# Kernel optimization log

Hardware: AMD Instinct MI355X
Metric: run time of the kernel (lower is better)

## Reference

```python
import jax, jax.numpy as jnp
import numpy as np

N, M, T = 8, 4, 500000   # state dim, measurement dim, trajectory length
ITERS = 100


def setup_inputs() -> dict:
    key = jax.random.key(0)
    k1, k2, k3, k4 = jax.random.split(key, 4)
    xs = jax.random.normal(k1, (N, T), dtype=jnp.float32)
    ys = jax.random.normal(k2, (M, T), dtype=jnp.float32)
    # Well-conditioned, stable models: F near identity, modest H, SPD noise covs.
    F = jnp.eye(N, dtype=jnp.float32) + 0.01 * jax.random.normal(k3, (N, N), dtype=jnp.float32)
    H = 0.1 * jax.random.normal(k4, (M, N), dtype=jnp.float32)
    Q = jnp.eye(N, dtype=jnp.float32)
    R = jnp.eye(M, dtype=jnp.float32)
    gamma = jnp.float32(0.01)
    return {"xs": xs, "ys": ys, "F": F, "H": H, "Q": Q, "R": R, "gamma": gamma}


def reference(xs, ys, F, H, Q, R, gamma):
    # Precompute the message operators (done once in __init__ in the original).
    Qinv = jnp.linalg.inv(Q)
    Rinv = jnp.linalg.inv(R)
    negQinv = -Qinv            # n x n
    FtQinv = F.T @ Qinv        # n x n
    HtRinv = H.T @ Rinv        # n x m

    def step(x, _):
        # x: n x T. Shift columns to get x_{t-1} and x_{t+1} (edge-replicated).
        x_past = jnp.concatenate([x[:, :1], x[:, :-1]], axis=1)
        x_fut = jnp.concatenate([x[:, 1:], x[:, -1:]], axis=1)
        # diff_past_curr: x_t - F x_{t-1}, with ROW 0 zeroed (faithful to res[0]=0.0)
        d1 = (x - F @ x_past).at[0].set(0.0)
        # diff_curr_fut: x_{t+1} - F x_t, with LAST ROW zeroed (faithful to res[-1]=0.0)
        d2 = (x_fut - F @ x).at[-1].set(0.0)
        # diff_y_curr: y - H x_t
        d3 = ys - H @ x
        m = negQinv @ d1 + FtQinv @ d2 + HtRinv @ d3
        return x + gamma * m, None

    x, _ = jax.lax.scan(step, xs, None, length=ITERS)
    return x
```

## Files before the change

### kernel.cpp

```cpp
#include <hip/hip_runtime.h>

#define TLEN   500000
#define NITER  100
#define DHALF  6
#define NOFF   (2*DHALF+1)
#define STRIP  20
#define EWIN   32
#define CT     256
#define CCPT   4
#define NCONV  (((TLEN - 2*STRIP)/CCPT + CT - 1) / CT)
#define WROW   128

__global__ __launch_bounds__(256) void band_and_edges(
    const float* __restrict__ xs, const float* __restrict__ ys,
    const float* __restrict__ F, const float* __restrict__ H,
    const float* __restrict__ Q, const float* __restrict__ R,
    const float* __restrict__ gam,
    float* __restrict__ wout,
    float* __restrict__ out)
{
  __shared__ double dQaug[8][16];
  __shared__ double dRaug[4][8];
  __shared__ double dFtQi[64], dHtRi[32], dA1[64], dB2[64];
  __shared__ float fmats[224];
  __shared__ __align__(16) float st[2][34][8];

  const int tid = threadIdx.x;
  const int b   = blockIdx.x;
  const int r8  = (tid >> 3) & 7;
  const int c8  = tid & 7;

  if (tid < 64) {
    dQaug[r8][c8]     = (double)Q[r8*8 + c8];
    dQaug[r8][c8 + 8] = (c8 == r8) ? 1.0 : 0.0;
  } else if (tid < 96) {
    int t = tid - 64, rr = t >> 3, cr = t & 7;
    dRaug[rr][cr] = (cr < 4) ? (double)R[rr*4 + cr] : ((cr - 4 == rr) ? 1.0 : 0.0);
  }
  __syncthreads();
  for (int col = 0; col < 8; ++col) {
    double piv = 1, fq = 0, p1 = 0, p2 = 0, m1 = 0, m2 = 0;
    double rpiv = 1, frr = 0, pr = 0, mr = 0;
    const bool doQ = tid < 64;
    const bool doR = (tid >= 64 && tid < 96 && col < 4);
    if (doQ) {
      piv = dQaug[col][col]; fq = dQaug[r8][col];
      p1 = dQaug[col][c8];   p2 = dQaug[col][c8 + 8];
      m1 = dQaug[r8][c8];    m2 = dQaug[r8][c8 + 8];
    }
    if (doR) {
      int t = tid - 64, rr = t >> 3, cr = t & 7;
      rpiv = dRaug[col][col]; frr = dRaug[rr][col];
      pr = dRaug[col][cr];    mr = dRaug[rr][cr];
    }
    __syncthreads();
    if (doQ) {
      dQaug[r8][c8]     = (r8 == col) ? m1 / piv : m1 - fq * (p1 / piv);
      dQaug[r8][c8 + 8] = (r8 == col) ? m2 / piv : m2 - fq * (p2 / piv);
    }
    if (doR) {
      int t = tid - 64, rr = t >> 3, cr = t & 7;
      dRaug[rr][cr] = (rr == col) ? mr / rpiv : mr - frr * (pr / rpiv);
    }
    __syncthreads();
  }
  if (tid < 64) {
    double s = 0.0;
    #pragma unroll
    for (int k = 0; k < 8; ++k) s += (double)F[k*8 + r8] * dQaug[k][c8 + 8];
    dFtQi[r8*8 + c8] = s;
    dA1[r8*8 + c8] = (c8 == 0) ? 0.0 : -dQaug[r8][c8 + 8];
  } else if (tid < 96) {
    int t = tid - 64, i = t >> 2, j = t & 3;
    double s = 0.0;
    #pragma unroll
    for (int k = 0; k < 4; ++k) s += (double)H[k*8 + i] * dRaug[k][j + 4];
    dHtRi[i*4 + j] = s;
  }
  __syncthreads();
  if (tid < 64) dB2[r8*8 + c8] = (c8 == 7) ? 0.0 : dFtQi[r8*8 + c8];
  __syncthreads();
  {
    const double g = (double)gam[0];
    if (tid < 64) {
      double sp = 0.0;
      #pragma unroll
      for (int k = 0; k < 8; ++k) sp -= dA1[r8*8 + k] * (double)F[k*8 + c8];
      double t2 = dA1[r8*8 + c8];
      #pragma unroll
      for (int k = 0; k < 8; ++k) t2 -= dB2[r8*8 + k] * (double)F[k*8 + c8];
      #pragma unroll
      for (int k = 0; k < 4; ++k) t2 -= dHtRi[r8*4 + k] * (double)H[k*8 + c8];
      fmats[       c8*8 + r8] = (float)(((r8 == c8) ? 1.0 : 0.0) + g * t2);
      fmats[ 64 +  c8*8 + r8] = (float)(g * sp);
      fmats[128 +  c8*8 + r8] = (float)(g * dB2[r8*8 + c8]);
    } else if (tid < 96) {
      int t = tid - 64, i = t >> 2, j = t & 3;
      fmats[192 + j*8 + i] = (float)(g * dHtRi[i*4 + j]);
    }
  }
  __syncthreads();

  const int i = tid & 7;
  const int g = tid >> 3;
  float cmr[8], pmr[8], fur[7];
  #pragma unroll
  for (int k = 0; k < 8; ++k) {
    cmr[k] = fmats[       k*8 + i];
    pmr[k] = fmats[ 64 +  k*8 + i];
    if (k < 7) fur[k] = fmats[128 + k*8 + i];
  }
  float* const stf = (float*)st;
  const int BUF = 34*8;

  if (b < 12) {
    const int c = b;
    const bool act = tid < NOFF*8;
    const int s = g + 1;
    for (int idx = tid; idx < 2*BUF; idx += 256) stf[idx] = 0.0f;
    __syncthreads();
    if (act && c < 8 && s == DHALF + 1 && i == c) st[0][s][i] = 1.0f;
    const float seed = (act && c >= 8 && s == DHALF + 1) ? fmats[192 + (c - 8)*8 + i] : 0.0f;
    __syncthreads();
    int p = 0;
    float last = 0.0f;
    #pragma unroll 1
    for (int it = 0; it < NITER; ++it) {
      if (act) {
        const float* sp_ = stf + p*BUF;
        const float4 o0 = *(const float4*)(sp_ + s*8);
        const float4 o1 = *(const float4*)(sp_ + s*8 + 4);
        const float4 u0 = *(const float4*)(sp_ + (s + 1)*8);
        const float4 u1 = *(const float4*)(sp_ + (s + 1)*8 + 4);
        const float4 d0 = *(const float4*)(sp_ + (s - 1)*8);
        const float4 d1 = *(const float4*)(sp_ + (s - 1)*8 + 4);
        float a0 = seed, a1 = 0.0f, a2 = 0.0f;
        a0 = fmaf(cmr[0], o0.x, a0); a0 = fmaf(cmr[1], o0.y, a0);
        a0 = fmaf(cmr[2], o0.z, a0); a0 = fmaf(cmr[3], o0.w, a0);
        a0 = fmaf(cmr[4], o1.x, a0); a0 = fmaf(cmr[5], o1.y, a0);
        a0 = fmaf(cmr[6], o1.z, a0); a0 = fmaf(cmr[7], o1.w, a0);
        a1 = fmaf(pmr[0], u0.x, a1); a1 = fmaf(pmr[1], u0.y, a1);
        a1 = fmaf(pmr[2], u0.z, a1); a1 = fmaf(pmr[3], u0.w, a1);
        a1 = fmaf(pmr[4], u1.x, a1); a1 = fmaf(pmr[5], u1.y, a1);
        a1 = fmaf(pmr[6], u1.z, a1); a1 = fmaf(pmr[7], u1.w, a1);
        a2 = fmaf(fur[0], d0.x, a2); a2 = fmaf(fur[1], d0.y, a2);
        a2 = fmaf(fur[2], d0.z, a2); a2 = fmaf(fur[3], d0.w, a2);
        a2 = fmaf(fur[4], d1.x, a2); a2 = fmaf(fur[5], d1.y, a2);
        a2 = fmaf(fur[6], d1.z, a2);
        last = a0 + a1 + a2;
        stf[(p^1)*BUF + s*8 + i] = last;
      }
      __syncthreads();
      p ^= 1;
    }
    if (act) wout[c*WROW + (s - 1)*8 + i] = last;
    if (tid >= NOFF*8 && tid < WROW) wout[c*WROW + tid] = 0.0f;
    return;
  }

  const bool left = (b == 12);
  const int col  = g;
  const int gcol = left ? col : (TLEN - EWIN + col);
  const int sL = (col > 0) ? col - 1 : 0;
  const int sR = (col < EWIN - 1) ? col + 1 : EWIN - 1;
  const float xv = xs[i*TLEN + gcol];
  float gyv;
  {
    gyv = fmats[192 +      i] * ys[0*TLEN + gcol];
    gyv = fmaf(fmats[192 +  8 + i], ys[1*TLEN + gcol], gyv);
    gyv = fmaf(fmats[192 + 16 + i], ys[2*TLEN + gcol], gyv);
    gyv = fmaf(fmats[192 + 24 + i], ys[3*TLEN + gcol], gyv);
  }
  st[0][col][i] = xv;
  __syncthreads();
  int p = 0;
  float last = xv;
  #pragma unroll 1
  for (int it = 0; it < NITER; ++it) {
    const float* sp_ = stf + p*BUF;
    const float4 o0 = *(const float4*)(sp_ + col*8);
    const float4 o1 = *(const float4*)(sp_ + col*8 + 4);
    const float4 l0 = *(const float4*)(sp_ + sL*8);
    const float4 l1 = *(const float4*)(sp_ + sL*8 + 4);
    const float4 q0 = *(const float4*)(sp_ + sR*8);
    const float4 q1 = *(const float4*)(sp_ + sR*8 + 4);
    float a0 = gyv, a1 = 0.0f, a2 = 0.0f;
    a0 = fmaf(cmr[0], o0.x, a0); a0 = fmaf(cmr[1], o0.y, a0);
    a0 = fmaf(cmr[2], o0.z, a0); a0 = fmaf(cmr[3], o0.w, a0);
    a0 = fmaf(cmr[4], o1.x, a0); a0 = fmaf(cmr[5], o1.y, a0);
    a0 = fmaf(cmr[6], o1.z, a0); a0 = fmaf(cmr[7], o1.w, a0);
    a1 = fmaf(pmr[0], l0.x, a1); a1 = fmaf(pmr[1], l0.y, a1);
    a1 = fmaf(pmr[2], l0.z, a1); a1 = fmaf(pmr[3], l0.w, a1);
    a1 = fmaf(pmr[4], l1.x, a1); a1 = fmaf(pmr[5], l1.y, a1);
    a1 = fmaf(pmr[6], l1.z, a1); a1 = fmaf(pmr[7], l1.w, a1);
    a2 = fmaf(fur[0], q0.x, a2); a2 = fmaf(fur[1], q0.y, a2);
    a2 = fmaf(fur[2], q0.z, a2); a2 = fmaf(fur[3], q0.w, a2);
    a2 = fmaf(fur[4], q1.x, a2); a2 = fmaf(fur[5], q1.y, a2);
    a2 = fmaf(fur[6], q1.z, a2);
    last = a0 + a1 + a2;
    stf[(p^1)*BUF + col*8 + i] = last;
    __syncthreads();
    p ^= 1;
  }
  if (left ? (col < STRIP) : (col >= EWIN - STRIP)) out[i*TLEN + gcol] = last;
}

__global__ __launch_bounds__(CT) void kgm_conv(
    const float* __restrict__ xs, const float* __restrict__ ys,
    const float* __restrict__ wq, float* __restrict__ out)
{
  const int tid  = threadIdx.x;
  const int lane = tid & 63;
  const int ocol = STRIP + (blockIdx.x * CT + tid) * CCPT;
  const int col0 = (ocol <= TLEN - STRIP - CCPT) ? ocol : (TLEN - STRIP - CCPT);

  float4 acc[8];
  #pragma unroll
  for (int i = 0; i < 8; ++i) acc[i] = make_float4(0.f, 0.f, 0.f, 0.f);

  #pragma unroll 2
  for (int k = 0; k < 12; ++k) {
    const float* src = ((k < 8) ? (xs + k*TLEN) : (ys + (k-8)*TLEN)) + col0;
    const float wA = wq[k*WROW + lane];
    const float wB = wq[k*WROW + 64 + lane];
    float z[20];
    #pragma unroll
    for (int j = 0; j < 5; ++j) {
      float4 v = *(const float4*)(src - 8 + 4*j);
      z[4*j] = v.x; z[4*j + 1] = v.y; z[4*j + 2] = v.z; z[4*j + 3] = v.w;
    }
    #pragma unroll
    for (int d = 0; d < NOFF; ++d) {
      #pragma unroll
      for (int i = 0; i < 8; ++i) {
        constexpr int dummy = 0; (void)dummy;
        const int j = d*8 + i;
        const int wi = __builtin_amdgcn_readlane(
            __float_as_int((j < 64) ? wA : wB), j & 63);
        const float w = __int_as_float(wi);
        acc[i].x = fmaf(w, z[d + 2], acc[i].x);
        acc[i].y = fmaf(w, z[d + 3], acc[i].y);
        acc[i].z = fmaf(w, z[d + 4], acc[i].z);
        acc[i].w = fmaf(w, z[d + 5], acc[i].w);
      }
    }
  }

  if (ocol < TLEN - STRIP) {
    #pragma unroll
    for (int i = 0; i < 8; ++i)
      *(float4*)(out + i*TLEN + ocol) = acc[i];
  }
}

extern "C" void kernel_launch(void* const* d_in, const int* in_sizes, int n_in,
                              void* d_out, int out_size, void* d_ws, size_t ws_size,
                              hipStream_t stream)
{
  (void)in_sizes; (void)n_in; (void)out_size; (void)ws_size;
  const float* xs = (const float*)d_in[0];
  const float* ys = (const float*)d_in[1];
  const float* F  = (const float*)d_in[2];
  const float* H  = (const float*)d_in[3];
  const float* Q  = (const float*)d_in[4];
  const float* R  = (const float*)d_in[5];
  const float* ga = (const float*)d_in[6];
  float* ws  = (float*)d_ws;
  float* out = (float*)d_out;
  band_and_edges<<<14, 256, 0, stream>>>(xs, ys, F, H, Q, R, ga, ws, out);
  kgm_conv<<<NCONV, CT, 0, stream>>>(xs, ys, ws, out);
}
```

Before: 49.95 us.

## Double-buffer row loads and read convolution weights as uniform scalar loads

```diff
diff --git a/kernel.cpp b/kernel.cpp
--- a/kernel.cpp
+++ b/kernel.cpp
@@ -210,7 +210,6 @@
     const float* __restrict__ wq, float* __restrict__ out)
 {
   const int tid  = threadIdx.x;
-  const int lane = tid & 63;
   const int ocol = STRIP + (blockIdx.x * CT + tid) * CCPT;
   const int col0 = (ocol <= TLEN - STRIP - CCPT) ? ocol : (TLEN - STRIP - CCPT);
 
@@ -218,33 +217,47 @@
   #pragma unroll
   for (int i = 0; i < 8; ++i) acc[i] = make_float4(0.f, 0.f, 0.f, 0.f);
 
-  #pragma unroll 2
-  for (int k = 0; k < 12; ++k) {
-    const float* src = ((k < 8) ? (xs + k*TLEN) : (ys + (k-8)*TLEN)) + col0;
-    const float wA = wq[k*WROW + lane];
-    const float wB = wq[k*WROW + 64 + lane];
-    float z[20];
-    #pragma unroll
-    for (int j = 0; j < 5; ++j) {
-      float4 v = *(const float4*)(src - 8 + 4*j);
-      z[4*j] = v.x; z[4*j + 1] = v.y; z[4*j + 2] = v.z; z[4*j + 3] = v.w;
-    }
-    #pragma unroll
-    for (int d = 0; d < NOFF; ++d) {
-      #pragma unroll
-      for (int i = 0; i < 8; ++i) {
-        constexpr int dummy = 0; (void)dummy;
-        const int j = d*8 + i;
-        const int wi = __builtin_amdgcn_readlane(
-            __float_as_int((j < 64) ? wA : wB), j & 63);
-        const float w = __int_as_float(wi);
-        acc[i].x = fmaf(w, z[d + 2], acc[i].x);
-        acc[i].y = fmaf(w, z[d + 3], acc[i].y);
-        acc[i].z = fmaf(w, z[d + 4], acc[i].z);
-        acc[i].w = fmaf(w, z[d + 5], acc[i].w);
-      }
-    }
-  }
+  float4 A[5], B[5];
+
+  #define LOADW(V, kk) { \
+    const float* s_ = (((kk) < 8) ? (xs + (kk)*TLEN) : (ys + ((kk)-8)*TLEN)) + col0; \
+    V[0] = *(const float4*)(s_ - 8); \
+    V[1] = *(const float4*)(s_ - 4); \
+    V[2] = *(const float4*)(s_); \
+    V[3] = *(const float4*)(s_ + 4); \
+    V[4] = *(const float4*)(s_ + 8); }
+
+  #define FMAK(V, kk) { \
+    const float z_[20] = {V[0].x,V[0].y,V[0].z,V[0].w, V[1].x,V[1].y,V[1].z,V[1].w, \
+                          V[2].x,V[2].y,V[2].z,V[2].w, V[3].x,V[3].y,V[3].z,V[3].w, \
+                          V[4].x,V[4].y,V[4].z,V[4].w}; \
+    const float* wk_ = wq + (kk)*WROW; \
+    _Pragma("unroll") \
+    for (int d = 0; d < NOFF; ++d) { \
+      _Pragma("unroll") \
+      for (int i = 0; i < 8; ++i) { \
+        const float w_ = wk_[d*8 + i]; \
+        acc[i].x = fmaf(w_, z_[d + 2], acc[i].x); \
+        acc[i].y = fmaf(w_, z_[d + 3], acc[i].y); \
+        acc[i].z = fmaf(w_, z_[d + 4], acc[i].z); \
+        acc[i].w = fmaf(w_, z_[d + 5], acc[i].w); \
+      } } }
+
+  LOADW(A, 0); LOADW(B, 1);
+  FMAK(A, 0);  LOADW(A, 2);
+  FMAK(B, 1);  LOADW(B, 3);
+  FMAK(A, 2);  LOADW(A, 4);
+  FMAK(B, 3);  LOADW(B, 5);
+  FMAK(A, 4);  LOADW(A, 6);
+  FMAK(B, 5);  LOADW(B, 7);
+  FMAK(A, 6);  LOADW(A, 8);
+  FMAK(B, 7);  LOADW(B, 9);
+  FMAK(A, 8);  LOADW(A, 10);
+  FMAK(B, 9);  LOADW(B, 11);
+  FMAK(A, 10);
+  FMAK(B, 11);
+  #undef LOADW
+  #undef FMAK
 
   if (ocol < TLEN - STRIP) {
     #pragma unroll
```

New measurement: 69.19 us. +38.5%, slower.
